# Kernel tuning notes

Hardware: AMD Instinct MI355X
Metric: run time of the kernel (lower is better)

The kernel has to match this reference:

```python
import jax, jax.numpy as jnp
import numpy as np


def setup_inputs() -> dict:
    key = jax.random.key(0)
    x = jax.random.normal(key, (8192, 32768), dtype=jnp.float32)
    return {"x": x, "k": 64}


def reference(x, k):
    # ReLU then keep only top-k values per row; everything else zeroed.
    x_relu = jax.nn.relu(x)
    kk = min(k, x.shape[-1])
    vals, idx = jax.lax.top_k(x_relu, kk)            # [B, k]
    rows = jnp.arange(x.shape[0])[:, None]           # [B, 1]
    out = jnp.zeros_like(x).at[rows, idx].set(vals)
    return out
```

## Files before the change

### kernel.cpp

```cpp
#include <hip/hip_runtime.h>
#include <stdint.h>


#define NT   1024
#define NCOL 32768
#define VPT  8
#define NB   2048
#define REP  2
#define LISTCAP 2048

__global__ __launch_bounds__(NT) void topk_select_kernel(
        const float* __restrict__ x, const int* __restrict__ kptr,
        float* __restrict__ out)
{
    __shared__ uint32_t hist[REP][NB];
    __shared__ uint32_t tielist[LISTCAP];
    __shared__ int s_found, s_B, s_kth, s_neq, s_cnt, s_cut;

    const int tid  = threadIdx.x;
    const int lane = tid & 63;
    const int wave = tid >> 6;
    const size_t base = (size_t)blockIdx.x * NCOL;

    int k = *kptr;
    if (k > NCOL) k = NCOL;

    const uint4* xv = (const uint4*)(x + base);
    uint4*       ov = (uint4*)(out + base);

    if (k <= 0) {
        #pragma unroll
        for (int j = 0; j < VPT; ++j)
            ov[j * NT + tid] = make_uint4(0u, 0u, 0u, 0u);
        return;
    }

    uint4 va[VPT];
    #pragma unroll
    for (int j = 0; j < VPT; ++j) va[j] = xv[j * NT + tid];
    #pragma unroll
    for (int j = 0; j < VPT; ++j) {
        uint32_t* p = (uint32_t*)&va[j];
        #pragma unroll
        for (int c = 0; c < 4; ++c) {
            uint32_t u = p[c];
            p[c] = ((int)u > 0) ? u : 0u;
        }
    }

    int kth = k;
    uint32_t prefix = 0u;
    uint32_t thr = 0u;
    int n_eq = 0;
    bool done = false;

    #pragma unroll
    for (int round = 0; round < 3; ++round) {
        for (int i = tid; i < REP * NB; i += NT)
            ((uint32_t*)hist)[i] = 0u;
        __syncthreads();

        if (!done) {
            const int r = wave & (REP - 1);
            #pragma unroll
            for (int j = 0; j < VPT; ++j) {
                const uint32_t* p = (const uint32_t*)&va[j];
                #pragma unroll
                for (int c = 0; c < 4; ++c) {
                    uint32_t vv = p[c];
                    bool act; uint32_t bin;
                    if (round == 0)      { act = (vv != 0u);                          bin = vv >> 21; }
                    else if (round == 1) { act = (vv != 0u) && ((vv >> 21) == prefix); bin = (vv >> 10) & 0x7FFu; }
                    else                 { act = (vv != 0u) && ((vv >> 10) == prefix); bin = vv & 0x3FFu; }
                    if (act) atomicAdd(&hist[r][bin], 1u);
                }
            }
        }
        __syncthreads();

        if (wave == 0) {
            uint32_t s = 0;
            for (int i = 0; i < 32; ++i) {
                int b = lane * 32 + ((i + lane) & 31);
                #pragma unroll
                for (int r2 = 0; r2 < REP; ++r2) s += hist[r2][b];
            }
            uint32_t suf = s;
            #pragma unroll
            for (int d = 1; d < 64; d <<= 1) {
                uint32_t t2 = __shfl_down(suf, d);
                if (lane + d < 64) suf += t2;
            }
            uint32_t t1  = __shfl_down(suf, 1);
            uint32_t nxt = (lane == 63) ? 0u : t1;
            bool cond = (!done) && (suf >= (uint32_t)kth) && (nxt < (uint32_t)kth);
            unsigned long long mask = __ballot(cond);
            if (mask == 0ull) {
                if (lane == 0) s_found = 0;
            } else {
                int G = __ffsll(mask) - 1;
                uint32_t cntG = __shfl(nxt, G);
                uint32_t h2 = 0;
                if (lane < 32) {
                    int b = G * 32 + lane;
                    #pragma unroll
                    for (int r2 = 0; r2 < REP; ++r2) h2 += hist[r2][b];
                }
                uint32_t suf2 = h2;
                #pragma unroll
                for (int d = 1; d < 64; d <<= 1) {
                    uint32_t t2 = __shfl_down(suf2, d);
                    if (lane + d < 64) suf2 += t2;
                }
                uint32_t t3   = __shfl_down(suf2, 1);
                uint32_t nxt2 = (lane == 63) ? 0u : t3;
                uint32_t ts   = cntG + suf2;
                uint32_t tsn  = cntG + nxt2;
                bool cond2 = (lane < 32) && (ts >= (uint32_t)kth) && (tsn < (uint32_t)kth);
                unsigned long long m2 = __ballot(cond2);
                int l = __ffsll(m2) - 1;
                uint32_t ngt  = __shfl(tsn, l);
                uint32_t cbin = __shfl(suf2 - nxt2, l);
                if (lane == 0) {
                    s_found = 1;
                    s_B   = G * 32 + l;
                    s_kth = kth - (int)ngt;
                    s_neq = (int)cbin;
                }
            }
        }
        __syncthreads();

        if (!done) {
            if (!s_found) { done = true; thr = 0u; }
            else {
                int B = s_B;
                kth  = s_kth;
                n_eq = s_neq;
                if (round == 0)      prefix = (uint32_t)B;
                else if (round == 1) prefix = (prefix << 11) | (uint32_t)B;
                else                 thr    = (prefix << 10) | (uint32_t)B;
            }
        }
        __syncthreads();
    }

    if (tid == 0) s_cnt = 0;
    __syncthreads();
    const bool need_tb = (thr != 0u) && (n_eq != kth);
    if (need_tb) {
        #pragma unroll
        for (int j = 0; j < VPT; ++j) {
            const uint32_t* p = (const uint32_t*)&va[j];
            #pragma unroll
            for (int c = 0; c < 4; ++c) {
                if (p[c] == thr) {
                    int slot = atomicAdd(&s_cnt, 1);
                    if (slot < LISTCAP)
                        tielist[slot] = (uint32_t)(j * 4096 + tid * 4 + c);
                }
            }
        }
    }
    __syncthreads();
    if (need_tb && tid == 0) {
        int n = s_cnt; if (n > LISTCAP) n = LISTCAP;
        for (int i = 1; i < n; ++i) {
            uint32_t key = tielist[i]; int j2 = i - 1;
            while (j2 >= 0 && tielist[j2] > key) { tielist[j2 + 1] = tielist[j2]; --j2; }
            tielist[j2 + 1] = key;
        }
        s_cut = (kth >= 1 && kth <= n) ? (int)tielist[kth - 1] : 0x7FFFFFFF;
    }
    __syncthreads();
    const int idx_cut = need_tb ? s_cut : 0x7FFFFFFF;

    #pragma unroll
    for (int j = 0; j < VPT; ++j) {
        const uint32_t* p = (const uint32_t*)&va[j];
        uint4 o;
        uint32_t* q = (uint32_t*)&o;
        #pragma unroll
        for (int c = 0; c < 4; ++c) {
            uint32_t vv = p[c];
            int idx = j * 4096 + tid * 4 + c;
            bool keep = (vv > thr) || (thr != 0u && vv == thr && idx <= idx_cut);
            q[c] = keep ? vv : 0u;
        }
        ov[j * NT + tid] = o;
    }
}

extern "C" void kernel_launch(void* const* d_in, const int* in_sizes, int n_in,
                              void* d_out, int out_size, void* d_ws, size_t ws_size,
                              hipStream_t stream) {
    const float* x    = (const float*)d_in[0];
    const int*   kptr = (const int*)d_in[1];
    float*       out  = (float*)d_out;
    const int rows = in_sizes[0] / NCOL;
    topk_select_kernel<<<rows, NT, 0, stream>>>(x, kptr, out);
}
```

Before: 1.758 ms.

## Zero output early, scatter only kept values, exit radix rounds early

```diff
diff --git a/kernel.cpp b/kernel.cpp
--- a/kernel.cpp
+++ b/kernel.cpp
@@ -6,15 +6,14 @@
 #define NCOL 32768
 #define VPT  8
 #define NB   2048
-#define REP  2
-#define LISTCAP 2048
-
-__global__ __launch_bounds__(NT) void topk_select_kernel(
+#define REP  4
+#define LISTCAP 6144
+
+__global__ __launch_bounds__(NT, 8) void topk_select_kernel(
         const float* __restrict__ x, const int* __restrict__ kptr,
         float* __restrict__ out)
 {
     __shared__ uint32_t hist[REP][NB];
-    __shared__ uint32_t tielist[LISTCAP];
     __shared__ int s_found, s_B, s_kth, s_neq, s_cnt, s_cut;
 
     const int tid  = threadIdx.x;
@@ -22,16 +21,16 @@
     const int wave = tid >> 6;
     const size_t base = (size_t)blockIdx.x * NCOL;
 
-    int k = *kptr;
+    int k = kptr[0];
     if (k > NCOL) k = NCOL;
 
     const uint4* xv = (const uint4*)(x + base);
     uint4*       ov = (uint4*)(out + base);
+    const uint4  z4 = make_uint4(0u, 0u, 0u, 0u);
 
     if (k <= 0) {
         #pragma unroll
-        for (int j = 0; j < VPT; ++j)
-            ov[j * NT + tid] = make_uint4(0u, 0u, 0u, 0u);
+        for (int j = 0; j < VPT; ++j) ov[j * NT + tid] = z4;
         return;
     }
 
@@ -46,21 +45,25 @@
             uint32_t u = p[c];
             p[c] = ((int)u > 0) ? u : 0u;
         }
+        ov[j * NT + tid] = z4;
     }
 
     int kth = k;
     uint32_t prefix = 0u;
     uint32_t thr = 0u;
-    int n_eq = 0;
-    bool done = false;
-
-    #pragma unroll
+    uint32_t keep_min = 0u;
+    int mode = 0;
+
     for (int round = 0; round < 3; ++round) {
-        for (int i = tid; i < REP * NB; i += NT)
-            ((uint32_t*)hist)[i] = 0u;
-        __syncthreads();
-
-        if (!done) {
+        {
+            uint4* h4 = (uint4*)hist;
+            #pragma unroll
+            for (int i = 0; i < (REP * NB / 4) / NT; ++i)
+                h4[i * NT + tid] = z4;
+        }
+        __syncthreads();
+
+        {
             const int r = wave & (REP - 1);
             #pragma unroll
             for (int j = 0; j < VPT; ++j) {
@@ -69,7 +72,7 @@
                 for (int c = 0; c < 4; ++c) {
                     uint32_t vv = p[c];
                     bool act; uint32_t bin;
-                    if (round == 0)      { act = (vv != 0u);                          bin = vv >> 21; }
+                    if (round == 0)      { act = (vv != 0u);                           bin = vv >> 21; }
                     else if (round == 1) { act = (vv != 0u) && ((vv >> 21) == prefix); bin = (vv >> 10) & 0x7FFu; }
                     else                 { act = (vv != 0u) && ((vv >> 10) == prefix); bin = vv & 0x3FFu; }
                     if (act) atomicAdd(&hist[r][bin], 1u);
@@ -78,13 +81,18 @@
         }
         __syncthreads();
 
+        #pragma unroll
+        for (int i = 0; i < NB / NT; ++i) {
+            int b = i * NT + tid;
+            hist[0][b] += hist[1][b] + hist[2][b] + hist[3][b];
+        }
+        __syncthreads();
+
         if (wave == 0) {
             uint32_t s = 0;
-            for (int i = 0; i < 32; ++i) {
-                int b = lane * 32 + ((i + lane) & 31);
-                #pragma unroll
-                for (int r2 = 0; r2 < REP; ++r2) s += hist[r2][b];
-            }
+            #pragma unroll 8
+            for (int i = 0; i < 32; ++i)
+                s += hist[0][lane * 32 + ((i + lane) & 31)];
             uint32_t suf = s;
             #pragma unroll
             for (int d = 1; d < 64; d <<= 1) {
@@ -93,19 +101,14 @@
             }
             uint32_t t1  = __shfl_down(suf, 1);
             uint32_t nxt = (lane == 63) ? 0u : t1;
-            bool cond = (!done) && (suf >= (uint32_t)kth) && (nxt < (uint32_t)kth);
+            bool cond = (suf >= (uint32_t)kth) && (nxt < (uint32_t)kth);
             unsigned long long mask = __ballot(cond);
             if (mask == 0ull) {
                 if (lane == 0) s_found = 0;
             } else {
                 int G = __ffsll(mask) - 1;
                 uint32_t cntG = __shfl(nxt, G);
-                uint32_t h2 = 0;
-                if (lane < 32) {
-                    int b = G * 32 + lane;
-                    #pragma unroll
-                    for (int r2 = 0; r2 < REP; ++r2) h2 += hist[r2][b];
-                }
+                uint32_t h2 = (lane < 32) ? hist[0][G * 32 + lane] : 0u;
                 uint32_t suf2 = h2;
                 #pragma unroll
                 for (int d = 1; d < 64; d <<= 1) {
@@ -131,24 +134,28 @@
         }
         __syncthreads();
 
-        if (!done) {
-            if (!s_found) { done = true; thr = 0u; }
-            else {
-                int B = s_B;
-                kth  = s_kth;
-                n_eq = s_neq;
-                if (round == 0)      prefix = (uint32_t)B;
-                else if (round == 1) prefix = (prefix << 11) | (uint32_t)B;
-                else                 thr    = (prefix << 10) | (uint32_t)B;
-            }
-        }
-        __syncthreads();
-    }
-
-    if (tid == 0) s_cnt = 0;
-    __syncthreads();
-    const bool need_tb = (thr != 0u) && (n_eq != kth);
-    if (need_tb) {
+        if (!s_found) { keep_min = 1u; mode = 0; break; }
+        kth = s_kth;
+        const int neq = s_neq;
+        const uint32_t B = (uint32_t)s_B;
+        if (round == 0) {
+            if (neq == kth) { keep_min = B << 21; mode = 0; break; }
+            prefix = B;
+        } else if (round == 1) {
+            if (neq == kth) { keep_min = ((prefix << 11) | B) << 10; mode = 0; break; }
+            prefix = (prefix << 11) | B;
+        } else {
+            thr = (prefix << 10) | B;
+            if (neq == kth) { keep_min = thr; mode = 0; }
+            else            { mode = 1; }
+        }
+    }
+
+    int idx_cut = 0x7FFFFFFF;
+    if (mode == 1) {
+        uint32_t* tielist = &hist[1][0];
+        if (tid == 0) s_cnt = 0;
+        __syncthreads();
         #pragma unroll
         for (int j = 0; j < VPT; ++j) {
             const uint32_t* p = (const uint32_t*)&va[j];
@@ -161,33 +168,33 @@
                 }
             }
         }
-    }
-    __syncthreads();
-    if (need_tb && tid == 0) {
-        int n = s_cnt; if (n > LISTCAP) n = LISTCAP;
-        for (int i = 1; i < n; ++i) {
-            uint32_t key = tielist[i]; int j2 = i - 1;
-            while (j2 >= 0 && tielist[j2] > key) { tielist[j2 + 1] = tielist[j2]; --j2; }
-            tielist[j2 + 1] = key;
-        }
-        s_cut = (kth >= 1 && kth <= n) ? (int)tielist[kth - 1] : 0x7FFFFFFF;
-    }
-    __syncthreads();
-    const int idx_cut = need_tb ? s_cut : 0x7FFFFFFF;
-
+        __syncthreads();
+        if (tid == 0) {
+            int n = s_cnt; if (n > LISTCAP) n = LISTCAP;
+            for (int i = 1; i < n; ++i) {
+                uint32_t key = tielist[i]; int j2 = i - 1;
+                while (j2 >= 0 && tielist[j2] > key) { tielist[j2 + 1] = tielist[j2]; --j2; }
+                tielist[j2 + 1] = key;
+            }
+            s_cut = (kth >= 1 && kth <= n) ? (int)tielist[kth - 1] : 0x7FFFFFFF;
+        }
+        __syncthreads();
+        idx_cut = s_cut;
+    }
+
+    __threadfence_block();
+    float* o = out + base;
     #pragma unroll
     for (int j = 0; j < VPT; ++j) {
         const uint32_t* p = (const uint32_t*)&va[j];
-        uint4 o;
-        uint32_t* q = (uint32_t*)&o;
         #pragma unroll
         for (int c = 0; c < 4; ++c) {
             uint32_t vv = p[c];
             int idx = j * 4096 + tid * 4 + c;
-            bool keep = (vv > thr) || (thr != 0u && vv == thr && idx <= idx_cut);
-            q[c] = keep ? vv : 0u;
-        }
-        ov[j * NT + tid] = o;
+            bool keep = (mode == 0) ? (vv >= keep_min && vv != 0u)
+                                    : (vv > thr || (vv == thr && idx <= idx_cut));
+            if (keep) o[idx] = __uint_as_float(vv);
+        }
     }
 }
 
```

Result: slower. 2.253 ms (+28.2%).
